# Optimization experiments

Measured on AMD Instinct MI355X. Metric: run time of the kernel, lower is better.

The kernel has to match this reference:

```python
import jax, jax.numpy as jnp
import numpy as np

D_IN = 256
D_OUT = 256

def setup_inputs() -> dict:
    key = jax.random.key(0)
    kx, kq, kk, kv = jax.random.split(key, 4)
    x = jax.random.normal(kx, (8, D_IN, 64, 64), dtype=jnp.float32)
    s = 1.0 / np.sqrt(D_IN)
    Wq = jax.random.normal(kq, (D_OUT, D_IN), dtype=jnp.float32) * s
    Wk = jax.random.normal(kk, (D_OUT, D_IN), dtype=jnp.float32) * s
    Wv = jax.random.normal(kv, (D_OUT, D_IN), dtype=jnp.float32) * s
    return {"x": x, "Wq": Wq, "Wk": Wk, "Wv": Wv}

def reference(x, Wq, Wk, Wv):
    b, c_in, h, w = x.shape
    c = Wq.shape[0]
    # 1x1 conv == channel linear; tokens along N = h*w
    xt = x.reshape(b, c_in, h * w).transpose(0, 2, 1)      # (b, N, c_in)
    q = jnp.einsum('bnc,dc->bnd', xt, Wq)                  # (b, N, c)
    k = jnp.einsum('bnc,dc->bnd', xt, Wk)
    v = jnp.einsum('bnc,dc->bnd', xt, Wv)
    wei = jnp.einsum('bnd,bmd->bnm', q, k) / jnp.sqrt(jnp.asarray(c, x.dtype))
    wei = jax.nn.softmax(wei, axis=-1)
    out = jnp.einsum('bnm,bmd->bnd', wei, v)               # (b, N, c)
    return out.transpose(0, 2, 1).reshape(b, c, h, w)
```

## Files before the change

### kernel.cpp

```cpp
#include <hip/hip_runtime.h>

#define DIN 256
#define NTOK 4096

typedef __bf16 bf16;
typedef __bf16 bf16x4 __attribute__((ext_vector_type(4)));
typedef __bf16 bf16x8 __attribute__((ext_vector_type(8)));
typedef float floatx16 __attribute__((ext_vector_type(16)));

__device__ inline floatx16 mfma32(bf16x8 a, bf16x8 b, floatx16 c) {
    return __builtin_amdgcn_mfma_f32_32x32x16_bf16(a, b, c, 0, 0, 0);
}

__device__ inline void async16(const void* g, void* l) {
    __builtin_amdgcn_global_load_lds(
        (const __attribute__((address_space(1))) unsigned int*)g,
        (__attribute__((address_space(3))) unsigned int*)l, 16, 0, 0);
}

__global__ void convert_w(const float* __restrict__ wq, const float* __restrict__ wk,
                          const float* __restrict__ wv, bf16* __restrict__ Wb) {
    int i = blockIdx.x * 256 + threadIdx.x;
    const float* src = (i < 65536) ? wq : (i < 131072 ? wk : wv);
    Wb[i] = (bf16)src[i & 65535];
}

__global__ __launch_bounds__(256, 2) void proj_kernel(
    const float* __restrict__ x, const bf16* __restrict__ Wb,
    bf16* __restrict__ Qo, bf16* __restrict__ Ko, bf16* __restrict__ Vo)
{
    __shared__ __attribute__((aligned(16))) char smem[33792 + 32768];
    bf16 (*xs)[264] = (bf16(*)[264])smem;
    bf16* bufB = (bf16*)smem;
    bf16* bufA = (bf16*)(smem + 33792);

    int bid = blockIdx.x;
    int b = bid & 7, nt = bid >> 3;
    int n0 = nt * 64;
    int t = threadIdx.x;
    int lane = t & 63, w = t >> 6;
    int l32 = lane & 31, h = lane >> 5;
    int hl = lane >> 5;
    int tokg = w >> 1;
    int og   = w & 1;

    int wofs[8];
#pragma unroll
    for (int jj = 0; jj < 8; ++jj) {
        int q = w * 8 + jj;
        int r2 = 2 * q + hl;
        int cs = (l32) ^ (r2 & 31);
        wofs[jj] = r2 * 512 + cs * 16;
    }

    {
        const float* xb = x + (size_t)b * DIN * NTOK;
#pragma unroll
        for (int it = 0; it < 16; ++it) {
            int flat = it * 256 + t;
            int c = flat >> 4;
            int nf = flat & 15;
            float4 v = *(const float4*)(xb + (size_t)c * NTOK + n0 + nf * 4);
            int nn = nf * 4;
            xs[nn + 0][c] = (bf16)v.x;
            xs[nn + 1][c] = (bf16)v.y;
            xs[nn + 2][c] = (bf16)v.z;
            xs[nn + 3][c] = (bf16)v.w;
        }
    }
    __syncthreads();

    {
        const char* src = (const char*)Wb;
#pragma unroll
        for (int jj = 0; jj < 8; ++jj)
            async16(src + wofs[jj], (char*)bufA + (w * 8 + jj) * 1024);
    }

    bf16x8 xf[16];
#pragma unroll
    for (int ks = 0; ks < 16; ++ks)
        xf[ks] = *(const bf16x8*)&xs[tokg * 32 + l32][ks * 16 + h * 8];

    __syncthreads();

    for (int p = 0; p < 12; ++p) {
        if (p < 11) {
            bf16* nb = ((p + 1) & 1) ? bufB : bufA;
            const char* src = (const char*)Wb + (size_t)(p + 1) * 32768;
#pragma unroll
            for (int jj = 0; jj < 8; ++jj)
                async16(src + wofs[jj], (char*)nb + (w * 8 + jj) * 1024);
        }

        const bf16* wb = (p & 1) ? bufB : bufA;
        const bf16* Wrd = wb + (og * 32 + l32) * 256;
        int mat = p >> 2, dg = p & 3;

        floatx16 acc;
#pragma unroll
        for (int i = 0; i < 16; ++i) acc[i] = 0.0f;

        if (mat < 2) {
#pragma unroll
            for (int ks = 0; ks < 16; ++ks) {
                bf16x8 wf = *(const bf16x8*)(Wrd + (((2 * ks + h) ^ l32) * 8));
                acc = mfma32(xf[ks], wf, acc);
            }
            bf16* Out = (mat == 0 ? Qo : Ko) + (size_t)b * NTOK * DIN;
            int d = dg * 64 + og * 32 + l32;
#pragma unroll
            for (int r = 0; r < 16; ++r) {
                int tok = n0 + tokg * 32 + (r & 3) + 8 * (r >> 2) + 4 * h;
                Out[(size_t)tok * DIN + d] = (bf16)acc[r];
            }
        } else {
#pragma unroll
            for (int ks = 0; ks < 16; ++ks) {
                bf16x8 wf = *(const bf16x8*)(Wrd + (((2 * ks + h) ^ l32) * 8));
                acc = mfma32(wf, xf[ks], acc);
            }
            bf16* Out = Vo + (size_t)b * DIN * NTOK;
            int tok = n0 + tokg * 32 + l32;
#pragma unroll
            for (int r = 0; r < 16; ++r) {
                int d = dg * 64 + og * 32 + (r & 3) + 8 * (r >> 2) + 4 * h;
                Out[(size_t)d * NTOK + tok] = (bf16)acc[r];
            }
        }
        __syncthreads();
    }
}

__global__ __launch_bounds__(512, 2) void attn_kernel(
    const bf16* __restrict__ Q, const bf16* __restrict__ K,
    const bf16* __restrict__ V, float* __restrict__ out)
{
    __shared__ bf16 Ks[2][64][256];
    __shared__ bf16 Vs[2][256][64];
    __shared__ bf16 Ps[2][128][64];

    int bid = blockIdx.x;
    int b = bid & 7, qt = bid >> 3;
    int n0 = qt * 128;
    int t = threadIdx.x, lane = t & 63, w = t >> 6;
    int l32 = lane & 31, h = lane >> 5;
    int lkey = (l32 & 7) ^ ((l32 >> 3) & 3);

    const bf16* Qb = Q + (size_t)b * NTOK * DIN;
    const bf16* Kb = K + (size_t)b * NTOK * DIN;
    const bf16* Vb = V + (size_t)b * DIN * NTOK;
    float* Lp = (float*)&Ps[0][0][0];

    if (w < 4) {
        int tokg = w >> 1, mg = w & 1;
        int krow = mg * 32 + l32;

        int koff[8];
#pragma unroll
        for (int jj = 0; jj < 8; ++jj) {
            int q = w * 8 + jj;
            int r = q * 2 + (lane >> 5);
            int ck = (lane & 31) ^ ((r & 7) ^ ((r >> 3) & 3));
            koff[jj] = (r * 256 + ck * 8) * 2;
        }

        bf16x8 qf[2][16];
#pragma unroll
        for (int ca = 0; ca < 2; ++ca) {
            const bf16* qrow = Qb + (size_t)(n0 + tokg * 64 + ca * 32 + l32) * DIN + h * 8;
#pragma unroll
            for (int ks = 0; ks < 16; ++ks) qf[ca][ks] = *(const bf16x8*)(qrow + ks * 16);
        }

        float lsum[2] = {0.0f, 0.0f};

#pragma unroll
        for (int jj = 0; jj < 8; ++jj) {
            async16((const char*)Kb + koff[jj], (bf16*)Ks[0] + (w * 8 + jj) * 512);
            async16((const char*)Kb + 32768 + koff[jj], (bf16*)Ks[1] + (w * 8 + jj) * 512);
        }
        __syncthreads();

        {
            const bf16* Krd = (const bf16*)Ks[0] + krow * 256;
            floatx16 st[2];
#pragma unroll
            for (int i = 0; i < 16; ++i) { st[0][i] = 0.0f; st[1][i] = 0.0f; }
#pragma unroll
            for (int ks = 0; ks < 16; ++ks) {
                bf16x8 kf = *(const bf16x8*)(Krd + (((2 * ks + h) ^ lkey) * 8));
                st[0] = mfma32(kf, qf[0][ks], st[0]);
                st[1] = mfma32(kf, qf[1][ks], st[1]);
            }
#pragma unroll
            for (int ca = 0; ca < 2; ++ca) {
                bf16* Prow = (bf16*)Ps[0] + (tokg * 64 + ca * 32 + l32) * 64;
                float tsum = 0.0f;
#pragma unroll
                for (int g = 0; g < 4; ++g) {
                    bf16x4 pk;
#pragma unroll
                    for (int i = 0; i < 4; ++i) {
                        float e = __expf(st[ca][g * 4 + i] * 0.0625f);
                        tsum += e;
                        pk[i] = (bf16)e;
                    }
                    *(bf16x4*)((char*)Prow + (((mg * 4 + g) ^ lkey) * 16) + h * 8) = pk;
                }
                lsum[ca] += tsum;
            }
        }
        __syncthreads();

        for (int mt = 0; mt < 64; ++mt) {
            if (mt < 62) {
                int kadd = (mt + 2) * 32768;
#pragma unroll
                for (int jj = 0; jj < 8; ++jj)
                    async16((const char*)Kb + kadd + koff[jj],
                            (bf16*)Ks[mt & 1] + (w * 8 + jj) * 512);
            }
            if (mt < 63) {
                const bf16* Krd = (const bf16*)Ks[(mt + 1) & 1] + krow * 256;
                floatx16 st[2];
#pragma unroll
                for (int i = 0; i < 16; ++i) { st[0][i] = 0.0f; st[1][i] = 0.0f; }
#pragma unroll
                for (int ks = 0; ks < 16; ++ks) {
                    bf16x8 kf = *(const bf16x8*)(Krd + (((2 * ks + h) ^ lkey) * 8));
                    st[0] = mfma32(kf, qf[0][ks], st[0]);
                    st[1] = mfma32(kf, qf[1][ks], st[1]);
                }
                bf16* Pw = (bf16*)Ps[(mt + 1) & 1];
#pragma unroll
                for (int ca = 0; ca < 2; ++ca) {
                    bf16* Prow = Pw + (tokg * 64 + ca * 32 + l32) * 64;
                    float tsum = 0.0f;
#pragma unroll
                    for (int g = 0; g < 4; ++g) {
                        bf16x4 pk;
#pragma unroll
                        for (int i = 0; i < 4; ++i) {
                            float e = __expf(st[ca][g * 4 + i] * 0.0625f);
                            tsum += e;
                            pk[i] = (bf16)e;
                        }
                        *(bf16x4*)((char*)Prow + (((mg * 4 + g) ^ lkey) * 16) + h * 8) = pk;
                    }
                    lsum[ca] += tsum;
                }
            }
            __syncthreads();
        }

#pragma unroll
        for (int ca = 0; ca < 2; ++ca) {
            float sv = lsum[ca];
            sv += __shfl_xor(sv, 32);
            if (h == 0) Lp[mg * 128 + tokg * 64 + ca * 32 + l32] = sv;
        }
        __syncthreads();
    } else {
        int slab = w - 4;

        int vofs[8];
#pragma unroll
        for (int jj = 0; jj < 8; ++jj) {
            int q = slab * 8 + jj;
            int d = q * 8 + (lane >> 3);
            int cv = (lane & 7) ^ ((d & 7) ^ ((d >> 3) & 3));
            vofs[jj] = (d * 4096 + cv * 8) * 2;
        }

        floatx16 oacc[8];
#pragma unroll
        for (int i = 0; i < 8; ++i)
            for (int j = 0; j < 16; ++j) oacc[i][j] = 0.0f;

#pragma unroll
        for (int jj = 0; jj < 8; ++jj)
            async16((const char*)Vb + vofs[jj], (bf16*)Vs[0] + (slab * 8 + jj) * 512);
        __syncthreads();
        __syncthreads();

        for (int mt = 0; mt < 64; ++mt) {
            if (mt < 63) {
                int vadd = (mt + 1) * 128;
#pragma unroll
                for (int jj = 0; jj < 8; ++jj)
                    async16((const char*)Vb + vadd + vofs[jj],
                            (bf16*)Vs[(mt + 1) & 1] + (slab * 8 + jj) * 512);
            }
            const bf16* Vrd = (const bf16*)Vs[mt & 1];
            const char* Prd = (const char*)Ps[mt & 1];
#pragma unroll
            for (int kst = 0; kst < 4; ++kst) {
                bf16x8 va[2], pb[4];
#pragma unroll
                for (int dc = 0; dc < 2; ++dc) {
                    int d = slab * 64 + dc * 32 + l32;
                    va[dc] = *(const bf16x8*)(Vrd + d * 64 + (((kst * 2 + h) ^ lkey) * 8));
                }
#pragma unroll
                for (int tc = 0; tc < 4; ++tc)
                    pb[tc] = *(const bf16x8*)(Prd + (tc * 32 + l32) * 128 +
                                              (((kst * 2 + h) ^ lkey) * 16));
#pragma unroll
                for (int dc = 0; dc < 2; ++dc)
#pragma unroll
                    for (int tc = 0; tc < 4; ++tc)
                        oacc[dc * 4 + tc] = mfma32(va[dc], pb[tc], oacc[dc * 4 + tc]);
            }
            __syncthreads();
        }

        __syncthreads();
        float* ob = out + (size_t)b * DIN * NTOK;
#pragma unroll
        for (int tc = 0; tc < 4; ++tc) {
            int tok = tc * 32 + l32;
            float rinv = 1.0f / (Lp[tok] + Lp[128 + tok]);
#pragma unroll
            for (int dc = 0; dc < 2; ++dc)
#pragma unroll
                for (int r = 0; r < 16; ++r) {
                    int d = slab * 64 + dc * 32 + (r & 3) + 8 * (r >> 2) + 4 * h;
                    ob[(size_t)d * NTOK + n0 + tok] = oacc[dc * 4 + tc][r] * rinv;
                }
        }
    }
}

extern "C" void kernel_launch(void* const* d_in, const int* in_sizes, int n_in,
                              void* d_out, int out_size, void* d_ws, size_t ws_size,
                              hipStream_t stream) {
    const float* x  = (const float*)d_in[0];
    const float* wq = (const float*)d_in[1];
    const float* wk = (const float*)d_in[2];
    const float* wv = (const float*)d_in[3];
    float* outf = (float*)d_out;

    char* ws = (char*)d_ws;
    bf16* Wb = (bf16*)(ws);
    bf16* Qp = (bf16*)(ws + (1u << 20));
    bf16* Kp = (bf16*)(ws + (1u << 20) + (16u << 20));
    bf16* Vp = (bf16*)(ws + (1u << 20) + (32u << 20));

    convert_w<<<768, 256, 0, stream>>>(wq, wk, wv, Wb);
    proj_kernel<<<512, 256, 0, stream>>>(x, Wb, Qp, Kp, Vp);
    attn_kernel<<<256, 512, 0, stream>>>(Qp, Kp, Vp, outf);
}
```

Before: 238.5 us.

## Load V fragments directly from global into registers and add MFMA priority hints

The PV warps now read V operands straight from global memory into double-buffered registers (vaA/vaB) instead of staging them through a shared-memory buffer with async copies, and the Vs LDS array is removed. The main loop is unrolled by two so each half uses a fixed P buffer and register set. s_setprio is raised around the MFMA runs in both the QK and PV warps to favour matrix issue. This cuts LDS footprint and LDS traffic, which could allow more resident blocks, but exposes global-load latency directly to the PV warps and raises register pressure.

```diff
diff --git a/kernel.cpp b/kernel.cpp
--- a/kernel.cpp
+++ b/kernel.cpp
@@ -137,7 +137,6 @@
     const bf16* __restrict__ V, float* __restrict__ out)
 {
     __shared__ bf16 Ks[2][64][256];
-    __shared__ bf16 Vs[2][256][64];
     __shared__ bf16 Ps[2][128][64];
 
     int bid = blockIdx.x;
@@ -187,12 +186,14 @@
             floatx16 st[2];
 #pragma unroll
             for (int i = 0; i < 16; ++i) { st[0][i] = 0.0f; st[1][i] = 0.0f; }
+            __builtin_amdgcn_s_setprio(1);
 #pragma unroll
             for (int ks = 0; ks < 16; ++ks) {
                 bf16x8 kf = *(const bf16x8*)(Krd + (((2 * ks + h) ^ lkey) * 8));
                 st[0] = mfma32(kf, qf[0][ks], st[0]);
                 st[1] = mfma32(kf, qf[1][ks], st[1]);
             }
+            __builtin_amdgcn_s_setprio(0);
 #pragma unroll
             for (int ca = 0; ca < 2; ++ca) {
                 bf16* Prow = (bf16*)Ps[0] + (tokg * 64 + ca * 32 + l32) * 64;
@@ -226,12 +227,14 @@
                 floatx16 st[2];
 #pragma unroll
                 for (int i = 0; i < 16; ++i) { st[0][i] = 0.0f; st[1][i] = 0.0f; }
+                __builtin_amdgcn_s_setprio(1);
 #pragma unroll
                 for (int ks = 0; ks < 16; ++ks) {
                     bf16x8 kf = *(const bf16x8*)(Krd + (((2 * ks + h) ^ lkey) * 8));
                     st[0] = mfma32(kf, qf[0][ks], st[0]);
                     st[1] = mfma32(kf, qf[1][ks], st[1]);
                 }
+                __builtin_amdgcn_s_setprio(0);
                 bf16* Pw = (bf16*)Ps[(mt + 1) & 1];
 #pragma unroll
                 for (int ca = 0; ca < 2; ++ca) {
@@ -264,55 +267,78 @@
     } else {
         int slab = w - 4;
 
-        int vofs[8];
-#pragma unroll
-        for (int jj = 0; jj < 8; ++jj) {
-            int q = slab * 8 + jj;
-            int d = q * 8 + (lane >> 3);
-            int cv = (lane & 7) ^ ((d & 7) ^ ((d >> 3) & 3));
-            vofs[jj] = (d * 4096 + cv * 8) * 2;
-        }
+        const bf16* Vr0 = Vb + (size_t)(slab * 64 + l32) * NTOK + h * 8;
+        const bf16* Vr1 = Vb + (size_t)(slab * 64 + 32 + l32) * NTOK + h * 8;
 
         floatx16 oacc[8];
 #pragma unroll
         for (int i = 0; i < 8; ++i)
             for (int j = 0; j < 16; ++j) oacc[i][j] = 0.0f;
 
-#pragma unroll
-        for (int jj = 0; jj < 8; ++jj)
-            async16((const char*)Vb + vofs[jj], (bf16*)Vs[0] + (slab * 8 + jj) * 512);
-        __syncthreads();
-        __syncthreads();
-
-        for (int mt = 0; mt < 64; ++mt) {
-            if (mt < 63) {
-                int vadd = (mt + 1) * 128;
-#pragma unroll
-                for (int jj = 0; jj < 8; ++jj)
-                    async16((const char*)Vb + vadd + vofs[jj],
-                            (bf16*)Vs[(mt + 1) & 1] + (slab * 8 + jj) * 512);
-            }
-            const bf16* Vrd = (const bf16*)Vs[mt & 1];
-            const char* Prd = (const char*)Ps[mt & 1];
-#pragma unroll
-            for (int kst = 0; kst < 4; ++kst) {
-                bf16x8 va[2], pb[4];
-#pragma unroll
-                for (int dc = 0; dc < 2; ++dc) {
-                    int d = slab * 64 + dc * 32 + l32;
-                    va[dc] = *(const bf16x8*)(Vrd + d * 64 + (((kst * 2 + h) ^ lkey) * 8));
-                }
-#pragma unroll
-                for (int tc = 0; tc < 4; ++tc)
-                    pb[tc] = *(const bf16x8*)(Prd + (tc * 32 + l32) * 128 +
-                                              (((kst * 2 + h) ^ lkey) * 16));
-#pragma unroll
-                for (int dc = 0; dc < 2; ++dc)
+        bf16x8 vaA[8], vaB[8];
+#pragma unroll
+        for (int kst = 0; kst < 4; ++kst) {
+            vaA[kst]     = *(const bf16x8*)(Vr0 + kst * 16);
+            vaA[4 + kst] = *(const bf16x8*)(Vr1 + kst * 16);
+        }
+        __syncthreads();
+        __syncthreads();
+
+#pragma unroll 1
+        for (int mt2 = 0; mt2 < 32; ++mt2) {
+            int mt = mt2 * 2;
+            {
+                int nn = (mt + 1) * 64;
+#pragma unroll
+                for (int kst = 0; kst < 4; ++kst) {
+                    vaB[kst]     = *(const bf16x8*)(Vr0 + nn + kst * 16);
+                    vaB[4 + kst] = *(const bf16x8*)(Vr1 + nn + kst * 16);
+                }
+                const char* Prd = (const char*)Ps[0];
+#pragma unroll
+                for (int kst = 0; kst < 4; ++kst) {
+                    bf16x8 pb[4];
 #pragma unroll
                     for (int tc = 0; tc < 4; ++tc)
-                        oacc[dc * 4 + tc] = mfma32(va[dc], pb[tc], oacc[dc * 4 + tc]);
-            }
-            __syncthreads();
+                        pb[tc] = *(const bf16x8*)(Prd + (tc * 32 + l32) * 128 +
+                                                  (((kst * 2 + h) ^ lkey) * 16));
+                    __builtin_amdgcn_s_setprio(1);
+#pragma unroll
+                    for (int tc = 0; tc < 4; ++tc) {
+                        oacc[tc]     = mfma32(vaA[kst],     pb[tc], oacc[tc]);
+                        oacc[4 + tc] = mfma32(vaA[4 + kst], pb[tc], oacc[4 + tc]);
+                    }
+                    __builtin_amdgcn_s_setprio(0);
+                }
+                __syncthreads();
+            }
+            {
+                if (mt2 < 31) {
+                    int nn = (mt + 2) * 64;
+#pragma unroll
+                    for (int kst = 0; kst < 4; ++kst) {
+                        vaA[kst]     = *(const bf16x8*)(Vr0 + nn + kst * 16);
+                        vaA[4 + kst] = *(const bf16x8*)(Vr1 + nn + kst * 16);
+                    }
+                }
+                const char* Prd = (const char*)Ps[1];
+#pragma unroll
+                for (int kst = 0; kst < 4; ++kst) {
+                    bf16x8 pb[4];
+#pragma unroll
+                    for (int tc = 0; tc < 4; ++tc)
+                        pb[tc] = *(const bf16x8*)(Prd + (tc * 32 + l32) * 128 +
+                                                  (((kst * 2 + h) ^ lkey) * 16));
+                    __builtin_amdgcn_s_setprio(1);
+#pragma unroll
+                    for (int tc = 0; tc < 4; ++tc) {
+                        oacc[tc]     = mfma32(vaB[kst],     pb[tc], oacc[tc]);
+                        oacc[4 + tc] = mfma32(vaB[4 + kst], pb[tc], oacc[4 + tc]);
+                    }
+                    __builtin_amdgcn_s_setprio(0);
+                }
+                __syncthreads();
+            }
         }
 
         __syncthreads();
```

Result: slower. 243.5 us (+2.1%).

## Enlarge projection tiles to 128 tokens and 128 output channels per step

Applied to the files above, without the earlier changes.

The projection kernel now runs 512 threads per block over 128 tokens and stages 128 weight rows per pipeline step, so it does 6 steps instead of 12. Each wave computes two 32x32 accumulators, reusing its x fragments across more MFMAs. The goal is fewer weight-tile reloads per token and fewer barriers. In exchange it uses 128 KB of LDS, which limits occupancy to one block per CU and halves the grid to 256 blocks.

```diff
diff --git a/kernel.cpp b/kernel.cpp
--- a/kernel.cpp
+++ b/kernel.cpp
@@ -25,22 +25,21 @@
     Wb[i] = (bf16)src[i & 65535];
 }
 
-__global__ __launch_bounds__(256, 2) void proj_kernel(
+__global__ __launch_bounds__(512, 2) void proj_kernel(
     const float* __restrict__ x, const bf16* __restrict__ Wb,
     bf16* __restrict__ Qo, bf16* __restrict__ Ko, bf16* __restrict__ Vo)
 {
-    __shared__ __attribute__((aligned(16))) char smem[33792 + 32768];
+    __shared__ __attribute__((aligned(16))) char smem[131072];
     bf16 (*xs)[264] = (bf16(*)[264])smem;
-    bf16* bufB = (bf16*)smem;
-    bf16* bufA = (bf16*)(smem + 33792);
+    bf16* bufA = (bf16*)smem;
+    bf16* bufB = (bf16*)(smem + 65536);
 
     int bid = blockIdx.x;
     int b = bid & 7, nt = bid >> 3;
-    int n0 = nt * 64;
+    int n0 = nt * 128;
     int t = threadIdx.x;
     int lane = t & 63, w = t >> 6;
     int l32 = lane & 31, h = lane >> 5;
-    int hl = lane >> 5;
     int tokg = w >> 1;
     int og   = w & 1;
 
@@ -48,8 +47,8 @@
 #pragma unroll
     for (int jj = 0; jj < 8; ++jj) {
         int q = w * 8 + jj;
-        int r2 = 2 * q + hl;
-        int cs = (l32) ^ (r2 & 31);
+        int r2 = 2 * q + h;
+        int cs = l32 ^ (r2 & 31);
         wofs[jj] = r2 * 512 + cs * 16;
     }
 
@@ -57,9 +56,9 @@
         const float* xb = x + (size_t)b * DIN * NTOK;
 #pragma unroll
         for (int it = 0; it < 16; ++it) {
-            int flat = it * 256 + t;
-            int c = flat >> 4;
-            int nf = flat & 15;
+            int flat = it * 512 + t;
+            int c = flat >> 5;
+            int nf = flat & 31;
             float4 v = *(const float4*)(xb + (size_t)c * NTOK + n0 + nf * 4);
             int nn = nf * 4;
             xs[nn + 0][c] = (bf16)v.x;
@@ -70,63 +69,80 @@
     }
     __syncthreads();
 
+    bf16x8 xf[16];
+#pragma unroll
+    for (int ks = 0; ks < 16; ++ks)
+        xf[ks] = *(const bf16x8*)&xs[tokg * 32 + l32][ks * 16 + h * 8];
+
+    __syncthreads();
+
     {
         const char* src = (const char*)Wb;
 #pragma unroll
         for (int jj = 0; jj < 8; ++jj)
             async16(src + wofs[jj], (char*)bufA + (w * 8 + jj) * 1024);
     }
-
-    bf16x8 xf[16];
-#pragma unroll
-    for (int ks = 0; ks < 16; ++ks)
-        xf[ks] = *(const bf16x8*)&xs[tokg * 32 + l32][ks * 16 + h * 8];
-
     __syncthreads();
 
-    for (int p = 0; p < 12; ++p) {
-        if (p < 11) {
+    for (int p = 0; p < 6; ++p) {
+        if (p < 5) {
             bf16* nb = ((p + 1) & 1) ? bufB : bufA;
-            const char* src = (const char*)Wb + (size_t)(p + 1) * 32768;
+            const char* src = (const char*)Wb + (size_t)(p + 1) * 65536;
 #pragma unroll
             for (int jj = 0; jj < 8; ++jj)
                 async16(src + wofs[jj], (char*)nb + (w * 8 + jj) * 1024);
         }
 
         const bf16* wb = (p & 1) ? bufB : bufA;
-        const bf16* Wrd = wb + (og * 32 + l32) * 256;
-        int mat = p >> 2, dg = p & 3;
-
-        floatx16 acc;
-#pragma unroll
-        for (int i = 0; i < 16; ++i) acc[i] = 0.0f;
+        int mat = p >> 1, dhalf = p & 1;
+
+        floatx16 acc[2];
+#pragma unroll
+        for (int dc = 0; dc < 2; ++dc)
+#pragma unroll
+            for (int i = 0; i < 16; ++i) acc[dc][i] = 0.0f;
 
         if (mat < 2) {
 #pragma unroll
             for (int ks = 0; ks < 16; ++ks) {
-                bf16x8 wf = *(const bf16x8*)(Wrd + (((2 * ks + h) ^ l32) * 8));
-                acc = mfma32(xf[ks], wf, acc);
+#pragma unroll
+                for (int dc = 0; dc < 2; ++dc) {
+                    int row = og * 64 + dc * 32 + l32;
+                    bf16x8 wf = *(const bf16x8*)((const char*)wb + row * 512 +
+                                                 (((2 * ks + h) ^ (row & 31)) * 16));
+                    acc[dc] = mfma32(xf[ks], wf, acc[dc]);
+                }
             }
             bf16* Out = (mat == 0 ? Qo : Ko) + (size_t)b * NTOK * DIN;
-            int d = dg * 64 + og * 32 + l32;
-#pragma unroll
-            for (int r = 0; r < 16; ++r) {
-                int tok = n0 + tokg * 32 + (r & 3) + 8 * (r >> 2) + 4 * h;
-                Out[(size_t)tok * DIN + d] = (bf16)acc[r];
+#pragma unroll
+            for (int dc = 0; dc < 2; ++dc) {
+                int d = dhalf * 128 + og * 64 + dc * 32 + l32;
+#pragma unroll
+                for (int r = 0; r < 16; ++r) {
+                    int tok = n0 + tokg * 32 + (r & 3) + 8 * (r >> 2) + 4 * h;
+                    Out[(size_t)tok * DIN + d] = (bf16)acc[dc][r];
+                }
             }
         } else {
 #pragma unroll
             for (int ks = 0; ks < 16; ++ks) {
-                bf16x8 wf = *(const bf16x8*)(Wrd + (((2 * ks + h) ^ l32) * 8));
-                acc = mfma32(wf, xf[ks], acc);
+#pragma unroll
+                for (int dc = 0; dc < 2; ++dc) {
+                    int row = og * 64 + dc * 32 + l32;
+                    bf16x8 wf = *(const bf16x8*)((const char*)wb + row * 512 +
+                                                 (((2 * ks + h) ^ (row & 31)) * 16));
+                    acc[dc] = mfma32(wf, xf[ks], acc[dc]);
+                }
             }
             bf16* Out = Vo + (size_t)b * DIN * NTOK;
             int tok = n0 + tokg * 32 + l32;
 #pragma unroll
-            for (int r = 0; r < 16; ++r) {
-                int d = dg * 64 + og * 32 + (r & 3) + 8 * (r >> 2) + 4 * h;
-                Out[(size_t)d * NTOK + tok] = (bf16)acc[r];
-            }
+            for (int dc = 0; dc < 2; ++dc)
+#pragma unroll
+                for (int r = 0; r < 16; ++r) {
+                    int d = dhalf * 128 + og * 64 + dc * 32 + (r & 3) + 8 * (r >> 2) + 4 * h;
+                    Out[(size_t)d * NTOK + tok] = (bf16)acc[dc][r];
+                }
         }
         __syncthreads();
     }
@@ -348,6 +364,6 @@
     bf16* Vp = (bf16*)(ws + (1u << 20) + (32u << 20));
 
     convert_w<<<768, 256, 0, stream>>>(wq, wk, wv, Wb);
-    proj_kernel<<<512, 256, 0, stream>>>(x, Wb, Qp, Kp, Vp);
+    proj_kernel<<<256, 512, 0, stream>>>(x, Wb, Qp, Kp, Vp);
     attn_kernel<<<256, 512, 0, stream>>>(Qp, Kp, Vp, outf);
 }
```

Result: no change. 237.4 us (-0.5%).
